# Optimization experiments

Hardware: AMD Instinct MI355X
Metric: run time of the kernel (lower is better)

The kernel has to match this reference:

```python
import jax, jax.numpy as jnp
import numpy as np

NODELEN = 17949
N_NODES = 512
N_EDGES = 4096
H2 = 768
EMB = 128
IN_DIM = 2 * NODELEN


def _seg_mean(h, src, dst, n):
    # gather neighbor features and mean-reduce per destination node
    msg = h[src]                                   # [E, F]
    s = jax.ops.segment_sum(msg, dst, num_segments=n)
    deg = jax.ops.segment_sum(jnp.ones((src.shape[0],), h.dtype), dst, num_segments=n)
    return s / jnp.maximum(deg, 1.0)[:, None]


def setup_inputs() -> dict:
    key = jax.random.key(0)
    ks = jax.random.split(key, 12)
    s = 0.02
    return {
        "x": jax.random.normal(ks[0], (N_NODES, NODELEN), jnp.float32),
        "edge_src": jax.random.randint(ks[1], (N_EDGES,), 0, N_NODES),
        "edge_dst": jax.random.randint(ks[2], (N_EDGES,), 0, N_NODES),
        "W_e2": jax.random.normal(ks[3], (H2, IN_DIM), jnp.float32) * s,
        "b_e2": jnp.zeros((H2,), jnp.float32),
        "W_e3": jax.random.normal(ks[4], (EMB, H2), jnp.float32) * s,
        "b_e3": jnp.zeros((EMB,), jnp.float32),
        "W_d1": jax.random.normal(ks[5], (H2, EMB), jnp.float32) * s,
        "b_d1": jnp.zeros((H2,), jnp.float32),
        "W_d3": jax.random.normal(ks[6], (IN_DIM, H2), jnp.float32) * s,
        "b_d3": jnp.zeros((IN_DIM,), jnp.float32),
    }


def reference(x, edge_src, edge_dst, W_e2, b_e2, W_e3, b_e3, W_d1, b_d1, W_d3, b_d3):
    n = x.shape[0]
    # depth-2 recursive GraphSAGE mean aggregation; agg[0]=0 after each hop
    h1 = _seg_mean(x, edge_src, edge_dst, n).at[:, 0].set(0.0)
    h2 = _seg_mean(h1, edge_src, edge_dst, n).at[:, 0].set(0.0)
    emb = jnp.concatenate([x, h2], axis=1)           # [N, 2*NODELEN]
    emb = emb.at[:, 0].set(0.0).at[:, NODELEN].set(0.0)
    # AutoEncoder (eval mode: dropout is identity)
    h = jax.nn.relu(emb @ W_e2.T + b_e2)
    encoded = h @ W_e3.T + b_e3
    h = jax.nn.relu(encoded @ W_d1.T + b_d1)
    decoded = h @ W_d3.T + b_d3
    return encoded, decoded
```

## Files before the change

### kernel.cpp

```cpp
#include <hip/hip_runtime.h>
#include <hip/hip_bf16.h>

#define NODELEN 17949
#define NN 512
#define NE 4096
#define H2 768
#define EMB 128
#define IN_DIM (2 * NODELEN)
#define KP1 35904
#define KITERS1 561
#define SPLITS 24
#define KCHUNK1 24
#define FPAD 18048
#define RPAD4 35968

#define BM 128
#define BN 64
#define BK 64

typedef __bf16 bf16x8 __attribute__((ext_vector_type(8)));
typedef float f32x4 __attribute__((ext_vector_type(4)));

#define GPTR(p) ((const __attribute__((address_space(1))) void*)(p))
#define LPTR(p) ((__attribute__((address_space(3))) void*)(p))


__global__ void k_zero_int(int* p, int n) {
    int i = blockIdx.x * 256 + threadIdx.x;
    if (i < n) p[i] = 0;
}

__global__ void k_zero_f4(float4* p, int n4) {
    int i = blockIdx.x * 256 + threadIdx.x;
    if (i < n4) p[i] = make_float4(0.f, 0.f, 0.f, 0.f);
}

__global__ void k_deg(const int* __restrict__ dst, int* __restrict__ cnt) {
    int e = blockIdx.x * 256 + threadIdx.x;
    if (e < NE) atomicAdd(&cnt[dst[e]], 1);
}

__global__ void k_invdeg(const int* __restrict__ cnt, float* __restrict__ invdeg) {
    int i = blockIdx.x * 256 + threadIdx.x;
    if (i < NN) {
        int c = cnt[i];
        invdeg[i] = 1.0f / (float)(c > 1 ? c : 1);
    }
}

__global__ void k_scatter(const int* __restrict__ src, const int* __restrict__ dst,
                          const float* __restrict__ invdeg, float* __restrict__ A) {
    int e = blockIdx.x * 256 + threadIdx.x;
    if (e < NE) {
        int d = dst[e];
        atomicAdd(&A[(size_t)d * NN + src[e]], invdeg[d]);
    }
}

__global__ void k_a2(const float* __restrict__ A, __bf16* __restrict__ A2b) {
    int i = blockIdx.x;
    int t = threadIdx.x;
    __shared__ float row[NN];
    row[t] = A[(size_t)i * NN + t];
    row[t + 256] = A[(size_t)i * NN + 256 + t];
    __syncthreads();
    float a0 = 0.f, a1 = 0.f;
    for (int s = 0; s < NN; ++s) {
        float a = row[s];
        if (a != 0.f) {
            a0 += a * A[(size_t)s * NN + t];
            a1 += a * A[(size_t)s * NN + 256 + t];
        }
    }
    A2b[(size_t)i * NN + t] = (__bf16)a0;
    A2b[(size_t)i * NN + 256 + t] = (__bf16)a1;
}

__global__ void k_xt_emb(const float* __restrict__ x, __bf16* __restrict__ xT,
                         __bf16* __restrict__ embb) {
    __shared__ float t[64][65];
    int f0 = blockIdx.x * 64, s0 = blockIdx.y * 64;
    int tx = threadIdx.x & 63, ty = threadIdx.x >> 6;
#pragma unroll
    for (int r = 0; r < 16; ++r) {
        int f = f0 + tx;
        int s = s0 + ty * 16 + r;
        float v = (f < NODELEN) ? x[(size_t)s * NODELEN + f] : 0.f;
        t[ty * 16 + r][tx] = v;
        if (f < NODELEN)
            embb[(size_t)s * KP1 + f] = (__bf16)((f == 0) ? 0.f : v);
    }
    __syncthreads();
#pragma unroll
    for (int r = 0; r < 16; ++r) {
        int f = f0 + ty * 16 + r;
        if (f < FPAD) xT[(size_t)f * NN + s0 + tx] = (__bf16)t[tx][ty * 16 + r];
    }
}

__global__ void k_pad(__bf16* __restrict__ embb) {
    int i = blockIdx.x * 256 + threadIdx.x;
    const int PAD = KP1 - IN_DIM;
    if (i < NN * PAD) {
        int n = i / PAD, c = i % PAD;
        embb[(size_t)n * KP1 + IN_DIM + c] = (__bf16)0.f;
    }
}

__global__ void k_cvt(const float* __restrict__ src, __bf16* __restrict__ dst,
                      int R, int C, int Rpad, int Cpad) {
    int C8 = Cpad / 8;
    int idx = blockIdx.x * 256 + threadIdx.x;
    if (idx >= Rpad * C8) return;
    int r = idx / C8, c8 = (idx % C8) * 8;
    __align__(16) __bf16 o[8];
    if (r < R && c8 + 8 <= C) {
        const float2* p = (const float2*)(src + (size_t)r * C + c8);
#pragma unroll
        for (int j = 0; j < 4; ++j) {
            float2 f = p[j];
            o[2 * j] = (__bf16)f.x;
            o[2 * j + 1] = (__bf16)f.y;
        }
    } else {
#pragma unroll
        for (int j = 0; j < 8; ++j) {
            int c = c8 + j;
            o[j] = (r < R && c < C) ? (__bf16)src[(size_t)r * C + c] : (__bf16)0.f;
        }
    }
    *(uint4*)&dst[(size_t)r * Cpad + c8] = *(uint4*)o;
}


template <int EPI>
__device__ __forceinline__ void gemm_body(
        const __bf16* __restrict__ A, int lda,
        const __bf16* __restrict__ B, int ldb,
        int Nvalid, int kIters, int kChunk,
        float* __restrict__ Cf, int ldc, const float* __restrict__ bias,
        __bf16* __restrict__ Cb) {
    __shared__ __align__(16) __bf16 As[BM * BK];
    __shared__ __align__(16) __bf16 Bs[BN * BK];

    const int tid = threadIdx.x;

    const int gx = gridDim.x, gy = gridDim.y;
    const int nwg = gx * gy * (int)gridDim.z;
    const int fid = blockIdx.x + gx * (blockIdx.y + gy * blockIdx.z);
    const int q = nwg >> 3, r = nwg & 7;
    const int xcd = fid & 7, idx = fid >> 3;
    const int lid = (xcd < r) ? xcd * (q + 1) + idx
                              : r * (q + 1) + (xcd - r) * q + idx;
    const int m0 = (lid % gx) * BM;
    const int rem = lid / gx;
    const int n0 = (rem % gy) * BN;
    const int z = rem / gy;

    int it0 = z * kChunk;
    int it1 = it0 + kChunk;
    if (it1 > kIters) it1 = kIters;

    const int wave = tid >> 6;
    const int lane = tid & 63;
    const int wm = (wave & 1) * 64;
    const int wn = (wave >> 1) * 32;
    const int fl = lane & 15;
    const int fq = lane >> 4;

    const __bf16* Abase = A + (size_t)(m0 + (tid >> 3)) * lda + (tid & 7) * 8;
    const __bf16* Bbase = B + (size_t)(n0 + (tid >> 3)) * ldb + (tid & 7) * 8;
    char* AsW = (char*)As + wave * 1024;
    char* BsW = (char*)Bs + wave * 1024;

    f32x4 acc[4][2] = {};

    for (int it = it0; it < it1; ++it) {
        const __bf16* Ag = Abase + it * BK;
        const __bf16* Bg = Bbase + it * BK;
#pragma unroll
        for (int rr = 0; rr < 4; ++rr)
            __builtin_amdgcn_global_load_lds(
                GPTR(Ag + (size_t)rr * 32 * lda), LPTR(AsW + rr * 4096), 16, 0, 0);
#pragma unroll
        for (int rr = 0; rr < 2; ++rr)
            __builtin_amdgcn_global_load_lds(
                GPTR(Bg + (size_t)rr * 32 * ldb), LPTR(BsW + rr * 4096), 16, 0, 0);
        __syncthreads();

#pragma unroll
        for (int ks = 0; ks < 2; ++ks) {
            const int kk = ks * 32 + fq * 8;
            bf16x8 af[4], bfr[2];
#pragma unroll
            for (int i = 0; i < 4; ++i)
                af[i] = *(const bf16x8*)&As[(wm + i * 16 + fl) * BK + kk];
#pragma unroll
            for (int j = 0; j < 2; ++j)
                bfr[j] = *(const bf16x8*)&Bs[(wn + j * 16 + fl) * BK + kk];
#pragma unroll
            for (int i = 0; i < 4; ++i)
#pragma unroll
                for (int j = 0; j < 2; ++j)
                    acc[i][j] = __builtin_amdgcn_mfma_f32_16x16x32_bf16(
                        af[i], bfr[j], acc[i][j], 0, 0, 0);
        }
        __syncthreads();
    }

#pragma unroll
    for (int i = 0; i < 4; ++i) {
#pragma unroll
        for (int j = 0; j < 2; ++j) {
#pragma unroll
            for (int rr = 0; rr < 4; ++rr) {
                int m = m0 + wm + i * 16 + fq * 4 + rr;
                int n = n0 + wn + j * 16 + fl;
                float v = acc[i][j][rr];
                if (EPI == 0) {
                    Cf[((size_t)z * NN + m) * H2 + n] = v;
                } else if (EPI == 1) {
                    if (n < Nvalid) Cf[(size_t)m * ldc + n] = v + bias[n];
                } else {
                    if (n < Nvalid)
                        Cb[(size_t)m * KP1 + NODELEN + n] = (n == 0) ? (__bf16)0.f : (__bf16)v;
                }
            }
        }
    }
}

__global__ __launch_bounds__(256, 4) void k_gemm_h2(
        const __bf16* __restrict__ A2b, const __bf16* __restrict__ xTb,
        __bf16* __restrict__ embb) {
    gemm_body<2>(A2b, NN, xTb, NN, NODELEN, NN / BK, NN / BK,
                 (float*)nullptr, 0, (const float*)nullptr, embb);
}

__global__ __launch_bounds__(256, 4) void k_gemm_e2(
        const __bf16* __restrict__ embb, const __bf16* __restrict__ We2b,
        float* __restrict__ partials) {
    gemm_body<0>(embb, KP1, We2b, KP1, H2, KITERS1, KCHUNK1,
                 partials, 0, (const float*)nullptr, (__bf16*)nullptr);
}

__global__ __launch_bounds__(256, 4) void k_gemm_d3(
        const __bf16* __restrict__ hd_b, const __bf16* __restrict__ Wd3b,
        const float* __restrict__ b_d3, float* __restrict__ dec) {
    gemm_body<1>(hd_b, H2, Wd3b, H2, IN_DIM, H2 / BK, H2 / BK,
                 dec, IN_DIM, b_d3, (__bf16*)nullptr);
}

__global__ void k_reduce(const float* __restrict__ partials,
                         const float* __restrict__ bias, float* __restrict__ h) {
    const int T4 = NN * H2 / 4;
    int i4 = blockIdx.x * 256 + threadIdx.x;
    if (i4 >= T4) return;
    const float4* p = (const float4*)partials;
    float4 s = make_float4(0.f, 0.f, 0.f, 0.f);
#pragma unroll
    for (int zz = 0; zz < SPLITS; ++zz) {
        float4 v = p[(size_t)zz * T4 + i4];
        s.x += v.x; s.y += v.y; s.z += v.z; s.w += v.w;
    }
    const float4 b = *(const float4*)&bias[(i4 * 4) % H2];
    s.x += b.x; s.y += b.y; s.z += b.z; s.w += b.w;
    s.x = s.x > 0.f ? s.x : 0.f;
    s.y = s.y > 0.f ? s.y : 0.f;
    s.z = s.z > 0.f ? s.z : 0.f;
    s.w = s.w > 0.f ? s.w : 0.f;
    *(float4*)&h[(size_t)i4 * 4] = s;
}

__global__ void k_enc(const float* __restrict__ h, const float* __restrict__ W,
                      const float* __restrict__ b, float* __restrict__ out) {
    int m = blockIdx.x, e = threadIdx.x;
    const float4* hr = (const float4*)(h + (size_t)m * H2);
    const float4* wr = (const float4*)(W + (size_t)e * H2);
    float s = 0.f;
#pragma unroll 4
    for (int i = 0; i < H2 / 4; ++i) {
        float4 a = hr[i];
        float4 w = wr[i];
        s += a.x * w.x + a.y * w.y + a.z * w.z + a.w * w.w;
    }
    out[(size_t)m * EMB + e] = s + b[e];
}

__global__ void k_dec1(const float* __restrict__ enc, const float* __restrict__ W,
                       const float* __restrict__ b, __bf16* __restrict__ hd) {
    int m = blockIdx.x;
    __shared__ float er[EMB];
    if (threadIdx.x < EMB) er[threadIdx.x] = enc[(size_t)m * EMB + threadIdx.x];
    __syncthreads();
    for (int j = threadIdx.x; j < H2; j += 256) {
        const float4* wr = (const float4*)(W + (size_t)j * EMB);
        float s = 0.f;
#pragma unroll
        for (int i = 0; i < EMB / 4; ++i) {
            float4 w = wr[i];
            s += w.x * er[4 * i] + w.y * er[4 * i + 1] + w.z * er[4 * i + 2] +
                 w.w * er[4 * i + 3];
        }
        float v = s + b[j];
        hd[(size_t)m * H2 + j] = (__bf16)(v > 0.f ? v : 0.f);
    }
}


extern "C" void kernel_launch(void* const* d_in, const int* in_sizes, int n_in,
                              void* d_out, int out_size, void* d_ws, size_t ws_size,
                              hipStream_t stream) {
    const float* x = (const float*)d_in[0];
    const int* esrc = (const int*)d_in[1];
    const int* edst = (const int*)d_in[2];
    const float* W_e2 = (const float*)d_in[3];
    const float* b_e2 = (const float*)d_in[4];
    const float* W_e3 = (const float*)d_in[5];
    const float* b_e3 = (const float*)d_in[6];
    const float* W_d1 = (const float*)d_in[7];
    const float* b_d1 = (const float*)d_in[8];
    const float* W_d3 = (const float*)d_in[9];
    const float* b_d3 = (const float*)d_in[10];
    float* out = (float*)d_out;

    char* w = (char*)d_ws;
    auto alloc = [&](size_t bytes) {
        char* p = w;
        w += (bytes + 255) & ~(size_t)255;
        return p;
    };
    __bf16* embb = (__bf16*)alloc((size_t)NN * KP1 * 2);
    char* uni = (char*)alloc((size_t)SPLITS * NN * H2 * 4);
    __bf16* xTb = (__bf16*)uni;
    float* Adj = (float*)(uni + (size_t)FPAD * NN * 2);
    __bf16* A2b = (__bf16*)((char*)Adj + (size_t)NN * NN * 4);
    int* cnt = (int*)((char*)A2b + (size_t)NN * NN * 2);
    float* invdeg = (float*)((char*)cnt + 2048);
    float* partials = (float*)uni;
    char* Wbig = alloc((size_t)RPAD4 * H2 * 2);
    __bf16* We2b = (__bf16*)Wbig;
    __bf16* Wd3b = (__bf16*)Wbig;
    float* h = (float*)alloc((size_t)NN * H2 * 4);
    __bf16* hd_b = (__bf16*)alloc((size_t)NN * H2 * 2);

    k_zero_int<<<2, 256, 0, stream>>>(cnt, NN);
    k_zero_f4<<<256, 256, 0, stream>>>((float4*)Adj, NN * NN / 4);
    k_deg<<<NE / 256, 256, 0, stream>>>(edst, cnt);
    k_invdeg<<<2, 256, 0, stream>>>(cnt, invdeg);
    k_scatter<<<NE / 256, 256, 0, stream>>>(esrc, edst, invdeg, Adj);
    k_a2<<<NN, 256, 0, stream>>>(Adj, A2b);

    dim3 gxt(FPAD / 64, NN / 64);
    k_xt_emb<<<gxt, 256, 0, stream>>>(x, xTb, embb);
    k_pad<<<(NN * (KP1 - IN_DIM) + 255) / 256, 256, 0, stream>>>(embb);

    dim3 gh2(NN / BM, FPAD / BN, 1);
    k_gemm_h2<<<gh2, 256, 0, stream>>>(A2b, xTb, embb);

    k_cvt<<<(H2 * (KP1 / 8) + 255) / 256, 256, 0, stream>>>(
        W_e2, We2b, H2, IN_DIM, H2, KP1);

    dim3 g1(NN / BM, H2 / BN, SPLITS);
    k_gemm_e2<<<g1, 256, 0, stream>>>(embb, We2b, partials);

    k_cvt<<<(RPAD4 * (H2 / 8) + 255) / 256, 256, 0, stream>>>(
        W_d3, Wd3b, IN_DIM, H2, RPAD4, H2);

    k_reduce<<<(NN * H2 / 4 + 255) / 256, 256, 0, stream>>>(partials, b_e2, h);

    k_enc<<<NN, EMB, 0, stream>>>(h, W_e3, b_e3, out);

    k_dec1<<<NN, 256, 0, stream>>>(out, W_d1, b_d1, hd_b);

    dim3 g4(NN / BM, RPAD4 / BN, 1);
    k_gemm_d3<<<g4, 256, 0, stream>>>(hd_b, Wd3b, b_d3, out + (size_t)NN * EMB);
}
```

Before: 540.9 us.

## Double-buffer GEMM LDS tiles and XOR-swizzle layout to avoid bank conflicts

Shared GEMM body now keeps two LDS buffers for the A and B tiles. The global-to-LDS load of the next K tile is issued before the MFMA compute on the current tile, so memory latency overlaps with math. The LDS layout is also XOR-swizzled by row so that 16-byte fragment reads spread across banks. The larger LDS footprint leads to launch bounds dropping from 4 to 3 workgroups per CU, which lowers occupancy.

```diff
diff --git a/kernel.cpp b/kernel.cpp
--- a/kernel.cpp
+++ b/kernel.cpp
@@ -140,8 +140,8 @@
         int Nvalid, int kIters, int kChunk,
         float* __restrict__ Cf, int ldc, const float* __restrict__ bias,
         __bf16* __restrict__ Cb) {
-    __shared__ __align__(16) __bf16 As[BM * BK];
-    __shared__ __align__(16) __bf16 Bs[BN * BK];
+    __shared__ __align__(16) __bf16 As[2][BM * BK];
+    __shared__ __align__(16) __bf16 Bs[2][BN * BK];
 
     const int tid = threadIdx.x;
 
@@ -167,37 +167,50 @@
     const int wn = (wave >> 1) * 32;
     const int fl = lane & 15;
     const int fq = lane >> 4;
-
-    const __bf16* Abase = A + (size_t)(m0 + (tid >> 3)) * lda + (tid & 7) * 8;
-    const __bf16* Bbase = B + (size_t)(n0 + (tid >> 3)) * ldb + (tid & 7) * 8;
-    char* AsW = (char*)As + wave * 1024;
-    char* BsW = (char*)Bs + wave * 1024;
+    const int fsw = fl & 7;
+
+    const int gslot = (tid & 7) ^ ((tid >> 3) & 7);
+    const __bf16* Abase = A + (size_t)(m0 + (tid >> 3)) * lda + gslot * 8;
+    const __bf16* Bbase = B + (size_t)(n0 + (tid >> 3)) * ldb + gslot * 8;
+    char* AsW0 = (char*)As[0] + wave * 1024;
+    char* BsW0 = (char*)Bs[0] + wave * 1024;
+    char* AsW1 = (char*)As[1] + wave * 1024;
+    char* BsW1 = (char*)Bs[1] + wave * 1024;
 
     f32x4 acc[4][2] = {};
 
-    for (int it = it0; it < it1; ++it) {
+    auto STAGE = [&](int it, int b) {
         const __bf16* Ag = Abase + it * BK;
         const __bf16* Bg = Bbase + it * BK;
+        char* aw = b ? AsW1 : AsW0;
+        char* bw = b ? BsW1 : BsW0;
 #pragma unroll
         for (int rr = 0; rr < 4; ++rr)
             __builtin_amdgcn_global_load_lds(
-                GPTR(Ag + (size_t)rr * 32 * lda), LPTR(AsW + rr * 4096), 16, 0, 0);
+                GPTR(Ag + (size_t)rr * 32 * lda), LPTR(aw + rr * 4096), 16, 0, 0);
 #pragma unroll
         for (int rr = 0; rr < 2; ++rr)
             __builtin_amdgcn_global_load_lds(
-                GPTR(Bg + (size_t)rr * 32 * ldb), LPTR(BsW + rr * 4096), 16, 0, 0);
-        __syncthreads();
-
+                GPTR(Bg + (size_t)rr * 32 * ldb), LPTR(bw + rr * 4096), 16, 0, 0);
+    };
+
+    auto COMPUTE = [&](int b) {
+        const __bf16* as = As[b];
+        const __bf16* bs = Bs[b];
 #pragma unroll
         for (int ks = 0; ks < 2; ++ks) {
-            const int kk = ks * 32 + fq * 8;
+            const int slot = (ks << 2) | fq;
             bf16x8 af[4], bfr[2];
 #pragma unroll
-            for (int i = 0; i < 4; ++i)
-                af[i] = *(const bf16x8*)&As[(wm + i * 16 + fl) * BK + kk];
-#pragma unroll
-            for (int j = 0; j < 2; ++j)
-                bfr[j] = *(const bf16x8*)&Bs[(wn + j * 16 + fl) * BK + kk];
+            for (int i = 0; i < 4; ++i) {
+                const int row = wm + i * 16 + fl;
+                af[i] = *(const bf16x8*)&as[row * BK + ((slot ^ fsw) << 3)];
+            }
+#pragma unroll
+            for (int j = 0; j < 2; ++j) {
+                const int row = wn + j * 16 + fl;
+                bfr[j] = *(const bf16x8*)&bs[row * BK + ((slot ^ fsw) << 3)];
+            }
 #pragma unroll
             for (int i = 0; i < 4; ++i)
 #pragma unroll
@@ -205,8 +218,21 @@
                     acc[i][j] = __builtin_amdgcn_mfma_f32_16x16x32_bf16(
                         af[i], bfr[j], acc[i][j], 0, 0, 0);
         }
+    };
+
+    if (it0 < it1) STAGE(it0, 0);
+    __syncthreads();
+    int it = it0;
+    while (it + 2 <= it1) {
+        STAGE(it + 1, 1);
+        COMPUTE(0);
         __syncthreads();
-    }
+        if (it + 2 < it1) STAGE(it + 2, 0);
+        COMPUTE(1);
+        __syncthreads();
+        it += 2;
+    }
+    if (it < it1) COMPUTE(0);
 
 #pragma unroll
     for (int i = 0; i < 4; ++i) {
@@ -230,21 +256,21 @@
     }
 }
 
-__global__ __launch_bounds__(256, 4) void k_gemm_h2(
+__global__ __launch_bounds__(256, 3) void k_gemm_h2(
         const __bf16* __restrict__ A2b, const __bf16* __restrict__ xTb,
         __bf16* __restrict__ embb) {
     gemm_body<2>(A2b, NN, xTb, NN, NODELEN, NN / BK, NN / BK,
                  (float*)nullptr, 0, (const float*)nullptr, embb);
 }
 
-__global__ __launch_bounds__(256, 4) void k_gemm_e2(
+__global__ __launch_bounds__(256, 3) void k_gemm_e2(
         const __bf16* __restrict__ embb, const __bf16* __restrict__ We2b,
         float* __restrict__ partials) {
     gemm_body<0>(embb, KP1, We2b, KP1, H2, KITERS1, KCHUNK1,
                  partials, 0, (const float*)nullptr, (__bf16*)nullptr);
 }
 
-__global__ __launch_bounds__(256, 4) void k_gemm_d3(
+__global__ __launch_bounds__(256, 3) void k_gemm_d3(
         const __bf16* __restrict__ hd_b, const __bf16* __restrict__ Wd3b,
         const float* __restrict__ b_d3, float* __restrict__ dec) {
     gemm_body<1>(hd_b, H2, Wd3b, H2, IN_DIM, H2 / BK, H2 / BK,
```

Result: no change. 547.1 us (+1.1%).
